# Optimization experiments

Measured on AMD Instinct MI355X. Metric: run time of the kernel, lower is better.

## Reference

```python
import jax, jax.numpy as jnp
import numpy as np

N, D = 8192, 64

def setup_inputs() -> dict:
    key = jax.random.key(0)
    sentence = jax.random.uniform(key, (N, D), dtype=jnp.float32)
    return {"sentence": sentence}

def reference(sentence):
    # weights[i, j] = <sentence[i], sentence[j]>  -> [n, n]
    weights = jnp.einsum('id,jd->ij', sentence, sentence)
    # sum-normalize each row (NOT softmax)
    weights = weights / jnp.sum(weights, axis=1, keepdims=True)
    # reweighted vectors: [n, n] @ [n, d] -> [n, d]
    return jnp.matmul(weights, sentence)
```

## Files before the change

### kernel.cpp

```cpp
#include <hip/hip_runtime.h>

#define N 8192
#define D 64
#define GRAM_BLOCKS 256
#define APPLY_BLOCKS 1024

__global__ __launch_bounds__(256) void gram_kernel(const float* __restrict__ S,
                                                   float* __restrict__ G,
                                                   float* __restrict__ t) {
    const int tid = threadIdx.x;
    const int ty = tid >> 4;
    const int tx = tid & 15;

    float acc[4][4];
#pragma unroll
    for (int i = 0; i < 4; ++i)
#pragma unroll
        for (int j = 0; j < 4; ++j) acc[i][j] = 0.f;
    float tac[4] = {0.f, 0.f, 0.f, 0.f};

    const int rpb = N / GRAM_BLOCKS;
    const int r0 = blockIdx.x * rpb;
    const float* Sa = S + (size_t)r0 * D + 4 * ty;
    const float* Sb = S + (size_t)r0 * D + 4 * tx;

#pragma unroll 8
    for (int r = 0; r < rpb; ++r) {
        const float4 a = *(const float4*)(Sa + (size_t)r * D);
        const float4 b = *(const float4*)(Sb + (size_t)r * D);
        const float av[4] = {a.x, a.y, a.z, a.w};
        const float bv[4] = {b.x, b.y, b.z, b.w};
#pragma unroll
        for (int i = 0; i < 4; ++i)
#pragma unroll
            for (int j = 0; j < 4; ++j) acc[i][j] += av[i] * bv[j];
        if (ty == 0) {
#pragma unroll
            for (int j = 0; j < 4; ++j) tac[j] += bv[j];
        }
    }

#pragma unroll
    for (int i = 0; i < 4; ++i)
#pragma unroll
        for (int j = 0; j < 4; ++j)
            atomicAdd(&G[(4 * ty + i) * D + 4 * tx + j], acc[i][j]);
    if (ty == 0) {
#pragma unroll
        for (int j = 0; j < 4; ++j) atomicAdd(&t[4 * tx + j], tac[j]);
    }
}

__global__ __launch_bounds__(256) void apply_kernel(const float* __restrict__ S,
                                                    const float* __restrict__ G,
                                                    const float* __restrict__ t,
                                                    float* __restrict__ out) {
    __shared__ float Gs[D * D];
    __shared__ float ts[D];
    const int tid = threadIdx.x;
#pragma unroll
    for (int i = tid; i < (D * D) / 4; i += 256)
        ((float4*)Gs)[i] = ((const float4*)G)[i];
    if (tid < D) ts[tid] = t[tid];
    __syncthreads();

    const int lane = tid & 63;
    const int wid = tid >> 6;
    const float tl = ts[lane];

    const int ia = (blockIdx.x * 4 + wid) * 2;
    const int ib = ia + 1;
    const float va = S[(size_t)ia * D + lane];
    const float vb = S[(size_t)ib * D + lane];

    float pa = va * tl, pb = vb * tl;
#pragma unroll
    for (int s = 1; s < 64; s <<= 1) {
        pa += __shfl_xor(pa, s, 64);
        pb += __shfl_xor(pb, s, 64);
    }

    float aa = 0.f, ab = 0.f;
#pragma unroll
    for (int k = 0; k < D; ++k) {
        const float g = Gs[k * D + lane];
        aa += __shfl(va, k, 64) * g;
        ab += __shfl(vb, k, 64) * g;
    }
    out[(size_t)ia * D + lane] = aa / pa;
    out[(size_t)ib * D + lane] = ab / pb;
}

extern "C" void kernel_launch(void* const* d_in, const int* in_sizes, int n_in,
                              void* d_out, int out_size, void* d_ws, size_t ws_size,
                              hipStream_t stream) {
    const float* S = (const float*)d_in[0];
    float* out = (float*)d_out;
    float* G = (float*)d_ws;
    float* t = G + D * D;

    hipMemsetAsync(d_ws, 0, (D * D + D) * sizeof(float), stream);
    gram_kernel<<<GRAM_BLOCKS, 256, 0, stream>>>(S, G, t);
    apply_kernel<<<APPLY_BLOCKS, 256, 0, stream>>>(S, G, t, out);
}
```

Before: 103.1 us.

## Replace atomic Gram accumulation with per-block partials and a separate reduction

```diff
diff --git a/kernel.cpp b/kernel.cpp
--- a/kernel.cpp
+++ b/kernel.cpp
@@ -2,12 +2,12 @@
 
 #define N 8192
 #define D 64
-#define GRAM_BLOCKS 256
-#define APPLY_BLOCKS 1024
+#define P 64
+#define SLICE (D * D + D)
+#define SLICE4 (SLICE / 4)
 
-__global__ __launch_bounds__(256) void gram_kernel(const float* __restrict__ S,
-                                                   float* __restrict__ G,
-                                                   float* __restrict__ t) {
+__global__ __launch_bounds__(256) void gram_partial(const float* __restrict__ S,
+                                                    float* __restrict__ ws) {
     const int tid = threadIdx.x;
     const int ty = tid >> 4;
     const int tx = tid & 15;
@@ -19,7 +19,7 @@
         for (int j = 0; j < 4; ++j) acc[i][j] = 0.f;
     float tac[4] = {0.f, 0.f, 0.f, 0.f};
 
-    const int rpb = N / GRAM_BLOCKS;
+    const int rpb = N / P;
     const int r0 = blockIdx.x * rpb;
     const float* Sa = S + (size_t)r0 * D + 4 * ty;
     const float* Sb = S + (size_t)r0 * D + 4 * tx;
@@ -40,14 +40,28 @@
         }
     }
 
+    float* pw = ws + (size_t)blockIdx.x * SLICE;
 #pragma unroll
     for (int i = 0; i < 4; ++i)
-#pragma unroll
-        for (int j = 0; j < 4; ++j)
-            atomicAdd(&G[(4 * ty + i) * D + 4 * tx + j], acc[i][j]);
-    if (ty == 0) {
-#pragma unroll
-        for (int j = 0; j < 4; ++j) atomicAdd(&t[4 * tx + j], tac[j]);
+        *(float4*)(pw + (4 * ty + i) * D + 4 * tx) =
+            make_float4(acc[i][0], acc[i][1], acc[i][2], acc[i][3]);
+    if (ty == 0)
+        *(float4*)(pw + D * D + 4 * tx) =
+            make_float4(tac[0], tac[1], tac[2], tac[3]);
+}
+
+__global__ __launch_bounds__(256) void reduce_kernel(float* __restrict__ ws) {
+    const float4* src = (const float4*)ws;
+    float4* dst = (float4*)(ws + (size_t)P * SLICE);
+    const int gid = blockIdx.x * 256 + threadIdx.x;
+    for (int i4 = gid; i4 < SLICE4; i4 += 1024) {
+        float4 acc = make_float4(0.f, 0.f, 0.f, 0.f);
+#pragma unroll 8
+        for (int p = 0; p < P; ++p) {
+            const float4 v = src[(size_t)p * SLICE4 + i4];
+            acc.x += v.x; acc.y += v.y; acc.z += v.z; acc.w += v.w;
+        }
+        dst[i4] = acc;
     }
 }
 
@@ -96,10 +110,11 @@
                               hipStream_t stream) {
     const float* S = (const float*)d_in[0];
     float* out = (float*)d_out;
-    float* G = (float*)d_ws;
-    float* t = G + D * D;
+    float* ws = (float*)d_ws;
+    float* Gfin = ws + (size_t)P * SLICE;
+    float* tfin = Gfin + D * D;
 
-    hipMemsetAsync(d_ws, 0, (D * D + D) * sizeof(float), stream);
-    gram_kernel<<<GRAM_BLOCKS, 256, 0, stream>>>(S, G, t);
-    apply_kernel<<<APPLY_BLOCKS, 256, 0, stream>>>(S, G, t, out);
+    gram_partial<<<P, 256, 0, stream>>>(S, ws);
+    reduce_kernel<<<4, 256, 0, stream>>>(ws);
+    apply_kernel<<<1024, 256, 0, stream>>>(S, Gfin, tfin, out);
 }
```

New measurement: 85.12 us (median of 2 runs). -17.4%, faster.
